# Performance work log

Measured on AMD Instinct MI355X. Metric: run time of the kernel, lower is better.

The kernel has to match this reference:

```python
import jax, jax.numpy as jnp
import numpy as np

N, D, BS = 262144, 64, 12  # nodes, eigvec dim, graphs per batch


def setup_inputs() -> dict:
    key = jax.random.key(0)
    k1, k2, k3 = jax.random.split(key, 3)
    inp = jax.random.normal(k1, (N, D), dtype=jnp.float32)
    tgt = jax.random.normal(k2, (N, D), dtype=jnp.float32)
    batch = jnp.sort(jax.random.randint(k3, (N,), 0, BS)).astype(jnp.int64)
    return {"input": inp, "target": tgt, "batch": batch, "batch_size": BS}


def _sign_combinations(batch_size, dtype):
    # itertools.product([1, -1], repeat=batch_size): first row all +1, last all -1.
    idx = jnp.arange(2 ** batch_size)
    shifts = (batch_size - 1) - jnp.arange(batch_size)
    bits = (idx[:, None] >> shifts[None, :]) & 1  # 0 -> +1, 1 -> -1
    return (1 - 2 * bits).astype(dtype)  # [2^BS, BS]


def reference(input, target, batch, batch_size):
    combos = _sign_combinations(batch_size, input.dtype)  # [C, BS]
    # Per-combination loss sum((s*x - t)^2) = sum(x^2) + sum(t^2) - 2 * sum_g s_g * e_g
    # where e_g = sum over nodes in graph g of <x_i, t_i>. Same math, no [C, N, D] blowup.
    cross = jax.ops.segment_sum(jnp.sum(input * target, axis=1), batch,
                                num_segments=batch_size)  # [BS]
    const = jnp.sum(input * input) + jnp.sum(target * target)
    combined_loss = const - 2.0 * (combos @ cross)  # [C]
    loss_idx = jnp.argmin(combined_loss)
    signed = combos[loss_idx][batch][:, None]  # [N, 1]
    loss = jnp.sum((input * signed - target) ** 2)  # F.mse_loss reduction='sum'
    return loss
```

## Files before the change

kernel.cpp:

```cpp
#include <hip/hip_runtime.h>

#define NBINS 12
#define GRID1 2048
#define BLK 256
#define STRIDE (GRID1 * BLK)

typedef float f4 __attribute__((ext_vector_type(4)));

__device__ __forceinline__ float dot4(f4 a, f4 b) {
    return a.x * b.x + a.y * b.y + a.z * b.z + a.w * b.w;
}
__device__ __forceinline__ float sq4(f4 a) {
    return a.x * a.x + a.y * a.y + a.z * a.z + a.w * a.w;
}
__device__ __forceinline__ void red16_atomic(float p, int g, float* cross, int lane) {
    p += __shfl_xor(p, 1);
    p += __shfl_xor(p, 2);
    p += __shfl_xor(p, 4);
    p += __shfl_xor(p, 8);
    if ((lane & 15) == 0) atomicAdd(&cross[g], p);
}

__global__ __launch_bounds__(BLK) void umse_partial(
    const f4* __restrict__ x4, const f4* __restrict__ t4,
    const int* __restrict__ batch32, float* __restrict__ ws, int nNodes)
{
    __shared__ float cross_lds[NBINS];
    __shared__ float redA[BLK / 64];

    const int tid = threadIdx.x;
    const int lane = tid & 63;

    if (tid < NBINS) cross_lds[tid] = 0.0f;
    const int is64 = (batch32[nNodes - 1] == 0) ? 1 : 0;
    __syncthreads();

    const int total = nNodes * 16;
    float sumsq = 0.0f;
    const int base = blockIdx.x * BLK + tid;

    if (total == 8 * STRIDE) {
        float dots[8];
        int gs[8];
        #pragma unroll
        for (int k = 0; k < 8; k += 4) {
            f4 a[4], b[4];
            #pragma unroll
            for (int j = 0; j < 4; ++j) {
                const int i = base + (k + j) * STRIDE;
                a[j] = __builtin_nontemporal_load(x4 + i);
                b[j] = __builtin_nontemporal_load(t4 + i);
            }
            #pragma unroll
            for (int j = 0; j < 4; ++j) {
                const int n = (base + (k + j) * STRIDE) >> 4;
                gs[k + j] = is64 ? batch32[n << 1] : batch32[n];
                sumsq += sq4(a[j]) + sq4(b[j]);
                dots[k + j] = dot4(a[j], b[j]);
            }
        }
        #pragma unroll
        for (int k = 0; k < 8; ++k)
            red16_atomic(dots[k], gs[k], cross_lds, lane);
    } else {
        const int nIter = total / STRIDE;
        int idx = base;
        for (int it = 0; it < nIter; ++it, idx += STRIDE) {
            f4 a = __builtin_nontemporal_load(x4 + idx);
            f4 b = __builtin_nontemporal_load(t4 + idx);
            const int n = idx >> 4;
            const int g = is64 ? batch32[n << 1] : batch32[n];
            sumsq += sq4(a) + sq4(b);
            red16_atomic(dot4(a, b), g, cross_lds, lane);
        }
        if (idx < total) {
            f4 a = x4[idx];
            f4 b = t4[idx];
            const int n = idx >> 4;
            const int g = is64 ? batch32[n << 1] : batch32[n];
            sumsq += sq4(a) + sq4(b);
            atomicAdd(&cross_lds[g], dot4(a, b));
        }
    }

    for (int m = 32; m; m >>= 1) sumsq += __shfl_xor(sumsq, m);
    if (lane == 0) redA[tid >> 6] = sumsq;
    __syncthreads();

    if (tid < NBINS) ws[tid * GRID1 + blockIdx.x] = cross_lds[tid];
    if (tid == NBINS) {
        float s = 0.0f;
        #pragma unroll
        for (int w = 0; w < BLK / 64; ++w) s += redA[w];
        ws[NBINS * GRID1 + blockIdx.x] = s;
    }
}

__global__ __launch_bounds__(832) void umse_final(
    const float* __restrict__ ws, float* __restrict__ out)
{
    __shared__ double cols[13];
    const int tid = threadIdx.x;
    const int w = tid >> 6, lane = tid & 63;

    double s = 0.0;
    for (int b = lane; b < GRID1; b += 64) s += (double)ws[w * GRID1 + b];
    for (int m = 32; m; m >>= 1) s += __shfl_xor(s, m);
    if (lane == 0) cols[w] = s;
    __syncthreads();

    if (tid == 0) {
        double acc = 0.0;
        for (int g = 0; g < NBINS; ++g) acc += fabs(cols[g]);
        out[0] = (float)(cols[12] - 2.0 * acc);
    }
}

extern "C" void kernel_launch(void* const* d_in, const int* in_sizes, int n_in,
                              void* d_out, int out_size, void* d_ws, size_t ws_size,
                              hipStream_t stream)
{
    const float* x = (const float*)d_in[0];
    const float* t = (const float*)d_in[1];
    const int* batch = (const int*)d_in[2];
    const int nNodes = in_sizes[2];
    float* ws = (float*)d_ws;
    float* out = (float*)d_out;

    umse_partial<<<GRID1, BLK, 0, stream>>>(
        (const f4*)x, (const f4*)t, batch, ws, nNodes);
    umse_final<<<1, 832, 0, stream>>>(ws, out);
}
```

Measured before the change: 154.2 us.

## Give each block a contiguous chunk with two float4 per thread per node

The fast path now assigns each block a contiguous range of PB float4s instead of a grid-strided pattern. Each lane loads two adjacent float4s per row, so a node's 16 float4s span 8 lanes, and the shuffle reduction drops to three steps. Batch ids are loaded up front, before the data loads. Launch bounds now request 4 blocks per SM. The intent is better DRAM locality and fewer shuffles and batch lookups, at the cost of more live registers per thread.

Result: no change. 156.6 us (+1.6%).

```diff
diff --git a/kernel.cpp b/kernel.cpp
--- a/kernel.cpp
+++ b/kernel.cpp
@@ -3,6 +3,7 @@
 #define NBINS 12
 #define GRID1 2048
 #define BLK 256
+#define PB 2048
 #define STRIDE (GRID1 * BLK)
 
 typedef float f4 __attribute__((ext_vector_type(4)));
@@ -13,15 +14,8 @@
 __device__ __forceinline__ float sq4(f4 a) {
     return a.x * a.x + a.y * a.y + a.z * a.z + a.w * a.w;
 }
-__device__ __forceinline__ void red16_atomic(float p, int g, float* cross, int lane) {
-    p += __shfl_xor(p, 1);
-    p += __shfl_xor(p, 2);
-    p += __shfl_xor(p, 4);
-    p += __shfl_xor(p, 8);
-    if ((lane & 15) == 0) atomicAdd(&cross[g], p);
-}
 
-__global__ __launch_bounds__(BLK) void umse_partial(
+__global__ __launch_bounds__(BLK, 4) void umse_partial(
     const f4* __restrict__ x4, const f4* __restrict__ t4,
     const int* __restrict__ batch32, float* __restrict__ ws, int nNodes)
 {
@@ -30,6 +24,7 @@
 
     const int tid = threadIdx.x;
     const int lane = tid & 63;
+    const int w = tid >> 6;
 
     if (tid < NBINS) cross_lds[tid] = 0.0f;
     const int is64 = (batch32[nNodes - 1] == 0) ? 1 : 0;
@@ -37,41 +32,57 @@
 
     const int total = nNodes * 16;
     float sumsq = 0.0f;
-    const int base = blockIdx.x * BLK + tid;
 
-    if (total == 8 * STRIDE) {
-        float dots[8];
-        int gs[8];
+    if (total == GRID1 * PB) {
+        const int start = blockIdx.x * PB;
+        const int wbase = start + w * 512;
+        const int tbase = wbase + lane * 2;
+        const int node0 = (start >> 4) + w * 32 + (lane >> 3);
+
+        int gs[4];
         #pragma unroll
-        for (int k = 0; k < 8; k += 4) {
-            f4 a[4], b[4];
-            #pragma unroll
-            for (int j = 0; j < 4; ++j) {
-                const int i = base + (k + j) * STRIDE;
-                a[j] = __builtin_nontemporal_load(x4 + i);
-                b[j] = __builtin_nontemporal_load(t4 + i);
-            }
-            #pragma unroll
-            for (int j = 0; j < 4; ++j) {
-                const int n = (base + (k + j) * STRIDE) >> 4;
-                gs[k + j] = is64 ? batch32[n << 1] : batch32[n];
-                sumsq += sq4(a[j]) + sq4(b[j]);
-                dots[k + j] = dot4(a[j], b[j]);
-            }
+        for (int r = 0; r < 4; ++r) {
+            const int n = node0 + r * 8;
+            gs[r] = is64 ? batch32[n << 1] : batch32[n];
+        }
+        f4 xa0[4], xa1[4], tb0[4], tb1[4];
+        #pragma unroll
+        for (int r = 0; r < 4; ++r) {
+            const int i = tbase + r * 128;
+            xa0[r] = __builtin_nontemporal_load(x4 + i);
+            xa1[r] = __builtin_nontemporal_load(x4 + i + 1);
+            tb0[r] = __builtin_nontemporal_load(t4 + i);
+            tb1[r] = __builtin_nontemporal_load(t4 + i + 1);
+        }
+        float dots[4];
+        #pragma unroll
+        for (int r = 0; r < 4; ++r) {
+            sumsq += sq4(xa0[r]) + sq4(xa1[r]) + sq4(tb0[r]) + sq4(tb1[r]);
+            dots[r] = dot4(xa0[r], tb0[r]) + dot4(xa1[r], tb1[r]);
         }
         #pragma unroll
-        for (int k = 0; k < 8; ++k)
-            red16_atomic(dots[k], gs[k], cross_lds, lane);
+        for (int r = 0; r < 4; ++r) {
+            float p = dots[r];
+            p += __shfl_xor(p, 1);
+            p += __shfl_xor(p, 2);
+            p += __shfl_xor(p, 4);
+            if ((lane & 7) == 0) atomicAdd(&cross_lds[gs[r]], p);
+        }
     } else {
         const int nIter = total / STRIDE;
-        int idx = base;
+        int idx = blockIdx.x * BLK + tid;
         for (int it = 0; it < nIter; ++it, idx += STRIDE) {
             f4 a = __builtin_nontemporal_load(x4 + idx);
             f4 b = __builtin_nontemporal_load(t4 + idx);
             const int n = idx >> 4;
             const int g = is64 ? batch32[n << 1] : batch32[n];
             sumsq += sq4(a) + sq4(b);
-            red16_atomic(dot4(a, b), g, cross_lds, lane);
+            float p = dot4(a, b);
+            p += __shfl_xor(p, 1);
+            p += __shfl_xor(p, 2);
+            p += __shfl_xor(p, 4);
+            p += __shfl_xor(p, 8);
+            if ((lane & 15) == 0) atomicAdd(&cross_lds[g], p);
         }
         if (idx < total) {
             f4 a = x4[idx];
@@ -91,7 +102,7 @@
     if (tid == NBINS) {
         float s = 0.0f;
         #pragma unroll
-        for (int w = 0; w < BLK / 64; ++w) s += redA[w];
+        for (int k = 0; k < BLK / 64; ++k) s += redA[k];
         ws[NBINS * GRID1 + blockIdx.x] = s;
     }
 }
```
